# Performance work log

Hardware: AMD Instinct MI355X
Metric: run time of the kernel (lower is better)

Reference implementation:

```python
import math
import jax, jax.numpy as jnp
import numpy as np

N_HEADS = 16


def setup_inputs() -> dict:
    key = jax.random.key(0)
    k1, k2 = jax.random.split(key)
    qkv = jax.random.normal(k1, (2, 3072, 2048), dtype=jnp.float32)
    mask = jax.random.randint(k2, (2, 1, 2048), 0, 2).astype(jnp.bool_)
    return {"qkv": qkv, "mask": mask}


def reference(qkv, mask):
    bs, width, length = qkv.shape
    ch = width // (3 * N_HEADS)
    q, k, v = jnp.split(qkv, 3, axis=1)  # each [bs, H*C, T]
    scale = 1.0 / math.sqrt(math.sqrt(ch))  # applied to both q and k
    q = (q * scale).reshape(bs * N_HEADS, ch, length)
    k = (k * scale).reshape(bs * N_HEADS, ch, length)
    # [B*H, T, T] scores
    weight = jnp.einsum('bct,bcs->bts', q, k)
    # mask: [bs, 1, T] bool, True = valid token
    inv = ~mask[:, 0, :]                      # [bs, T]
    pad = inv[:, None, :] | inv[:, :, None]   # [bs, T, T]
    pad = jnp.broadcast_to(pad[:, None], (bs, N_HEADS, length, length))
    pad = pad.reshape(bs * N_HEADS, length, length)
    weight = jnp.where(pad, jnp.finfo(weight.dtype).min, weight)
    weight = jax.nn.softmax(weight.astype(jnp.float32), axis=-1).astype(qkv.dtype)
    a = jnp.einsum('bts,bcs->bct', weight, v.reshape(bs * N_HEADS, ch, length))
    return a.reshape(bs, N_HEADS * ch, length)
```

## Files before the change

kernel.cpp:

```cpp
#include <hip/hip_runtime.h>
#include <float.h>


typedef __attribute__((ext_vector_type(8))) short bf16x8;
typedef __attribute__((ext_vector_type(4))) float f32x4;

#define TSEQ 2048
#define QT_OFF 0L
#define KT_OFF 4194304L
#define VB_OFF 8388608L

#if __has_builtin(__builtin_amdgcn_exp2f)
#define EXPFN(x) __builtin_amdgcn_exp2f(x)
#define SM_SCALE (0.125f * 1.44269504088896f)
#else
#define EXPFN(x) __expf(x)
#define SM_SCALE 0.125f
#endif

__device__ inline short f2bf(float x) {
    union { float f; unsigned u; } un; un.f = x;
    unsigned r = un.u + 0x7fffu + ((un.u >> 16) & 1u);
    return (short)(r >> 16);
}

__device__ inline unsigned pkbf(float a, float b) {
    unsigned au = __float_as_uint(a) + 0x8000u;
    unsigned bu = __float_as_uint(b) + 0x8000u;
    return __builtin_amdgcn_perm(bu, au, 0x07060302u);
}

__global__ __launch_bounds__(256) void prep_kernel(
    const float* __restrict__ qkv, short* __restrict__ ws)
{
    const int tid = threadIdx.x;
    const int job = blockIdx.x;
    if (job < 2048) {
        __shared__ float Ls[64 * 65];
        const int which = job & 1;
        const int rest  = job >> 1;
        const int bh = rest & 31;
        const int tt = rest >> 5;
        const int b = bh >> 4, h = bh & 15;
        const float* src = qkv + (long)b * 6291456 + ((long)(which * 1024 + h * 64)) * TSEQ + tt * 64;
        short* dst = ws + (which ? KT_OFF : QT_OFF) + ((long)bh * TSEQ + tt * 64) * 64;
        const float scale = which ? 1.0f : SM_SCALE;
        #pragma unroll
        for (int ch = 0; ch < 4; ++ch) {
            int idx = tid + ch * 256;
            int c = idx >> 4, tch = idx & 15;
            float4 v = *(const float4*)(src + (long)c * TSEQ + tch * 4);
            float* L = &Ls[c * 65 + tch * 4];
            L[0] = v.x; L[1] = v.y; L[2] = v.z; L[3] = v.w;
        }
        __syncthreads();
        #pragma unroll
        for (int ch = 0; ch < 2; ++ch) {
            int idx = tid + ch * 256;
            int t = idx >> 3, cch = idx & 7;
            bf16x8 o;
            #pragma unroll
            for (int j = 0; j < 8; ++j)
                o[j] = f2bf(Ls[(cch * 8 + j) * 65 + t] * scale);
            *(bf16x8*)(dst + (long)t * 64 + cch * 8) = o;
        }
    } else {
        const int v = job - 2048;
        #pragma unroll
        for (int ch = 0; ch < 4; ++ch) {
            long i = (long)v * 4096 + tid * 4 + ch * 1024;
            long b = i >> 21, r = i & 2097151;
            float4 x = *(const float4*)(qkv + b * 6291456 + 4194304 + r);
            short4 o;
            o.x = f2bf(x.x); o.y = f2bf(x.y); o.z = f2bf(x.z); o.w = f2bf(x.w);
            *(short4*)(ws + VB_OFF + i) = o;
        }
    }
}

__global__ __launch_bounds__(256, 2) void attn_kernel(
    const short* __restrict__ ws, const int* __restrict__ mask,
    float* __restrict__ out)
{
    __shared__ __align__(16) char smem[63488];
    short* Ps  = (short*)smem;
    float* mbf = (float*)(smem + 55296);
    float* Os  = (float*)smem;

    const int tid  = threadIdx.x;
    const int lane = tid & 63, wid = tid >> 6;
    const int l15  = lane & 15, quad = lane >> 4;
    const int srow = tid >> 3, scch = tid & 7;

    const int blk  = blockIdx.x;
    const int head = blk & 31;
    const int qt   = blk >> 5;
    const int b    = head >> 4, h = head & 15;
    const int t0   = qt * 128;

    const short* Qt = ws + QT_OFF + (long)head * TSEQ * 64;
    const short* Kt = ws + KT_OFF + (long)head * TSEQ * 64;
    const short* Vg = ws + VB_OFF + (long)head * 64 * TSEQ;
    const long obase = ((long)b * 1024 + h * 64) * TSEQ;

    for (int i = tid; i < TSEQ; i += 256)
        mbf[i] = (mask[b * TSEQ + i] != 0) ? 0.0f : -1e30f;

    #pragma unroll
    for (int ch = 0; ch < 4; ++ch) {
        int row = srow + ch * 32;
        *(bf16x8*)&Ps[row * 72 + scch * 8] =
            *(const bf16x8*)(Qt + (long)(t0 + row) * 64 + scch * 8);
    }
    #pragma unroll
    for (int ch = 0; ch < 2; ++ch) {
        int row = srow + ch * 32;
        *(bf16x8*)(smem + 18432 + (row * 72 + scch * 8) * 2) =
            *(const bf16x8*)(Kt + (long)row * 64 + scch * 8);
        *(bf16x8*)(smem + 36864 + (row * 72 + scch * 8) * 2) =
            *(const bf16x8*)(Vg + (long)row * TSEQ + scch * 8);
    }
    __syncthreads();

    bf16x8 qb[2][2];
    #pragma unroll
    for (int nt = 0; nt < 2; ++nt)
        #pragma unroll
        for (int hf = 0; hf < 2; ++hf)
            qb[nt][hf] = *(const bf16x8*)&Ps[(wid * 32 + nt * 16 + l15) * 72 + quad * 8 + hf * 32];
    bool qv[2];
    #pragma unroll
    for (int nt = 0; nt < 2; ++nt)
        qv[nt] = (mbf[t0 + wid * 32 + nt * 16 + l15] != 0.0f);

    float l_s[2] = {0.0f, 0.0f};
    f32x4 Oacc[2][4];
    #pragma unroll
    for (int mt = 0; mt < 2; ++mt)
        #pragma unroll
        for (int nc = 0; nc < 4; ++nc)
            #pragma unroll
            for (int r = 0; r < 4; ++r) Oacc[mt][nc][r] = 0.0f;

    short* Pw = Ps + wid * 32 * 72;
    int p = 0;

    for (int it = 0; it < 32; ++it) {
        const int s0 = it * 64;
        const int sn = ((it + 1) & 31) * 64;
        short* Kb = (short*)(smem + 18432 + p * 9216);
        short* Vb = (short*)(smem + 36864 + p * 9216);
        short* Kn = (short*)(smem + 18432 + (1 - p) * 9216);
        short* Vn = (short*)(smem + 36864 + (1 - p) * 9216);

        bf16x8 kst[2], vst[2];
        #pragma unroll
        for (int ch = 0; ch < 2; ++ch) {
            int row = srow + ch * 32;
            kst[ch] = *(const bf16x8*)(Kt + (long)(sn + row) * 64 + scch * 8);
            vst[ch] = *(const bf16x8*)(Vg + (long)row * TSEQ + sn + scch * 8);
        }

        f32x4 bias[4];
        #pragma unroll
        for (int ns = 0; ns < 4; ++ns)
            bias[ns] = *(const f32x4*)&mbf[s0 + ns * 16 + quad * 4];

        f32x4 Sacc[4][2];
        #pragma unroll
        for (int ns = 0; ns < 4; ++ns) {
            bf16x8 ka0 = *(const bf16x8*)&Kb[(ns * 16 + l15) * 72 + quad * 8];
            bf16x8 ka1 = *(const bf16x8*)&Kb[(ns * 16 + l15) * 72 + quad * 8 + 32];
            #pragma unroll
            for (int nt = 0; nt < 2; ++nt) {
                Sacc[ns][nt] = __builtin_amdgcn_mfma_f32_16x16x32_bf16(
                    ka0, qb[nt][0], bias[ns], 0, 0, 0);
                Sacc[ns][nt] = __builtin_amdgcn_mfma_f32_16x16x32_bf16(
                    ka1, qb[nt][1], Sacc[ns][nt], 0, 0, 0);
            }
        }

        #pragma unroll
        for (int nt = 0; nt < 2; ++nt) {
            float ls = 0.0f;
            #pragma unroll
            for (int ns = 0; ns < 4; ++ns) {
                float pv[4];
                #pragma unroll
                for (int r = 0; r < 4; ++r) {
                    float e = EXPFN(Sacc[ns][nt][r]);
                    pv[r] = qv[nt] ? 1.0f : e;
                    ls += pv[r];
                }
                uint2 pk;
                pk.x = pkbf(pv[0], pv[1]);
                pk.y = pkbf(pv[2], pv[3]);
                *(uint2*)&Pw[(nt * 16 + l15) * 72 + ns * 16 + quad * 4] = pk;
            }
            ls += __shfl_xor(ls, 16);
            ls += __shfl_xor(ls, 32);
            l_s[nt] += ls;
        }

        bf16x8 pa[2][2];
        #pragma unroll
        for (int mt = 0; mt < 2; ++mt)
            #pragma unroll
            for (int hf = 0; hf < 2; ++hf)
                pa[mt][hf] = *(const bf16x8*)&Pw[(mt * 16 + l15) * 72 + quad * 8 + hf * 32];
        #pragma unroll
        for (int hf = 0; hf < 2; ++hf)
            #pragma unroll
            for (int nc = 0; nc < 4; ++nc) {
                bf16x8 vb = *(const bf16x8*)&Vb[(nc * 16 + l15) * 72 + quad * 8 + hf * 32];
                #pragma unroll
                for (int mt = 0; mt < 2; ++mt)
                    Oacc[mt][nc] = __builtin_amdgcn_mfma_f32_16x16x32_bf16(
                        pa[mt][hf], vb, Oacc[mt][nc], 0, 0, 0);
            }

        #pragma unroll
        for (int ch = 0; ch < 2; ++ch) {
            int row = srow + ch * 32;
            *(bf16x8*)&Kn[row * 72 + scch * 8] = kst[ch];
            *(bf16x8*)&Vn[row * 72 + scch * 8] = vst[ch];
        }
        __syncthreads();
        p ^= 1;
    }

    float inv[2];
    #pragma unroll
    for (int nt = 0; nt < 2; ++nt) inv[nt] = 1.0f / l_s[nt];
    float iw[2][4];
    #pragma unroll
    for (int mt = 0; mt < 2; ++mt)
        #pragma unroll
        for (int r = 0; r < 4; ++r)
            iw[mt][r] = __shfl(inv[mt], 4 * quad + r);
    #pragma unroll
    for (int mt = 0; mt < 2; ++mt)
        #pragma unroll
        for (int nc = 0; nc < 4; ++nc) {
            float4 o;
            o.x = Oacc[mt][nc][0] * iw[mt][0];
            o.y = Oacc[mt][nc][1] * iw[mt][1];
            o.z = Oacc[mt][nc][2] * iw[mt][2];
            o.w = Oacc[mt][nc][3] * iw[mt][3];
            *(float4*)&Os[(nc * 16 + l15) * 132 + wid * 32 + mt * 16 + quad * 4] = o;
        }
    __syncthreads();
    #pragma unroll
    for (int ch = 0; ch < 8; ++ch) {
        int idx = tid + ch * 256;
        int c = idx >> 5, tch = idx & 31;
        *(float4*)(out + obase + (long)c * TSEQ + t0 + tch * 4) =
            *(const float4*)&Os[c * 132 + tch * 4];
    }
}

extern "C" void kernel_launch(void* const* d_in, const int* in_sizes, int n_in,
                              void* d_out, int out_size, void* d_ws, size_t ws_size,
                              hipStream_t stream) {
    const float* qkv  = (const float*)d_in[0];
    const int*   mask = (const int*)d_in[1];
    float*       out  = (float*)d_out;
    short*       ws   = (short*)d_ws;
    prep_kernel<<<dim3(3072), dim3(256), 0, stream>>>(qkv, ws);
    attn_kernel<<<dim3(512), dim3(256), 0, stream>>>(ws, mask, out);
}
```

Baseline: 150.3 us.

## Load K/V MFMA fragments directly from global into registers, drop LDS staging

Removes the shared-memory double-buffered K and V tiles and the per-iteration block barrier. Each wave now reads its Q, K and V MFMA fragments straight from global memory into registers, with K for the next tile prefetched in registers. LDS use drops to the per-wave P scratch and the mask bias, which could allow more blocks per CU. In exchange every wave redundantly fetches the same K/V data from L1/L2 rather than sharing it through LDS. Register pressure also rises from holding the prefetched fragments.

```diff
diff --git a/kernel.cpp b/kernel.cpp
--- a/kernel.cpp
+++ b/kernel.cpp
@@ -82,15 +82,14 @@
     const short* __restrict__ ws, const int* __restrict__ mask,
     float* __restrict__ out)
 {
-    __shared__ __align__(16) char smem[63488];
+    __shared__ __align__(16) char smem[33792];
     short* Ps  = (short*)smem;
-    float* mbf = (float*)(smem + 55296);
+    float* mbf = (float*)(smem + 18432);
     float* Os  = (float*)smem;
 
     const int tid  = threadIdx.x;
     const int lane = tid & 63, wid = tid >> 6;
     const int l15  = lane & 15, quad = lane >> 4;
-    const int srow = tid >> 3, scch = tid & 7;
 
     const int blk  = blockIdx.x;
     const int head = blk & 31;
@@ -105,21 +104,6 @@
 
     for (int i = tid; i < TSEQ; i += 256)
         mbf[i] = (mask[b * TSEQ + i] != 0) ? 0.0f : -1e30f;
-
-    #pragma unroll
-    for (int ch = 0; ch < 4; ++ch) {
-        int row = srow + ch * 32;
-        *(bf16x8*)&Ps[row * 72 + scch * 8] =
-            *(const bf16x8*)(Qt + (long)(t0 + row) * 64 + scch * 8);
-    }
-    #pragma unroll
-    for (int ch = 0; ch < 2; ++ch) {
-        int row = srow + ch * 32;
-        *(bf16x8*)(smem + 18432 + (row * 72 + scch * 8) * 2) =
-            *(const bf16x8*)(Kt + (long)row * 64 + scch * 8);
-        *(bf16x8*)(smem + 36864 + (row * 72 + scch * 8) * 2) =
-            *(const bf16x8*)(Vg + (long)row * TSEQ + scch * 8);
-    }
     __syncthreads();
 
     bf16x8 qb[2][2];
@@ -127,7 +111,8 @@
     for (int nt = 0; nt < 2; ++nt)
         #pragma unroll
         for (int hf = 0; hf < 2; ++hf)
-            qb[nt][hf] = *(const bf16x8*)&Ps[(wid * 32 + nt * 16 + l15) * 72 + quad * 8 + hf * 32];
+            qb[nt][hf] = *(const bf16x8*)(Qt +
+                (long)(t0 + wid * 32 + nt * 16 + l15) * 64 + quad * 8 + hf * 32);
     bool qv[2];
     #pragma unroll
     for (int nt = 0; nt < 2; ++nt)
@@ -143,23 +128,33 @@
             for (int r = 0; r < 4; ++r) Oacc[mt][nc][r] = 0.0f;
 
     short* Pw = Ps + wid * 32 * 72;
-    int p = 0;
+
+    bf16x8 kf[4][2];
+    #pragma unroll
+    for (int ns = 0; ns < 4; ++ns)
+        #pragma unroll
+        for (int hf = 0; hf < 2; ++hf)
+            kf[ns][hf] = *(const bf16x8*)(Kt +
+                (long)(ns * 16 + l15) * 64 + quad * 8 + hf * 32);
 
     for (int it = 0; it < 32; ++it) {
         const int s0 = it * 64;
         const int sn = ((it + 1) & 31) * 64;
-        short* Kb = (short*)(smem + 18432 + p * 9216);
-        short* Vb = (short*)(smem + 36864 + p * 9216);
-        short* Kn = (short*)(smem + 18432 + (1 - p) * 9216);
-        short* Vn = (short*)(smem + 36864 + (1 - p) * 9216);
-
-        bf16x8 kst[2], vst[2];
-        #pragma unroll
-        for (int ch = 0; ch < 2; ++ch) {
-            int row = srow + ch * 32;
-            kst[ch] = *(const bf16x8*)(Kt + (long)(sn + row) * 64 + scch * 8);
-            vst[ch] = *(const bf16x8*)(Vg + (long)row * TSEQ + sn + scch * 8);
-        }
+
+        bf16x8 vf[4][2];
+        #pragma unroll
+        for (int nc = 0; nc < 4; ++nc)
+            #pragma unroll
+            for (int hf = 0; hf < 2; ++hf)
+                vf[nc][hf] = *(const bf16x8*)(Vg +
+                    (long)(nc * 16 + l15) * TSEQ + s0 + quad * 8 + hf * 32);
+        bf16x8 kn[4][2];
+        #pragma unroll
+        for (int ns = 0; ns < 4; ++ns)
+            #pragma unroll
+            for (int hf = 0; hf < 2; ++hf)
+                kn[ns][hf] = *(const bf16x8*)(Kt +
+                    (long)(sn + ns * 16 + l15) * 64 + quad * 8 + hf * 32);
 
         f32x4 bias[4];
         #pragma unroll
@@ -168,17 +163,14 @@
 
         f32x4 Sacc[4][2];
         #pragma unroll
-        for (int ns = 0; ns < 4; ++ns) {
-            bf16x8 ka0 = *(const bf16x8*)&Kb[(ns * 16 + l15) * 72 + quad * 8];
-            bf16x8 ka1 = *(const bf16x8*)&Kb[(ns * 16 + l15) * 72 + quad * 8 + 32];
+        for (int ns = 0; ns < 4; ++ns)
             #pragma unroll
             for (int nt = 0; nt < 2; ++nt) {
                 Sacc[ns][nt] = __builtin_amdgcn_mfma_f32_16x16x32_bf16(
-                    ka0, qb[nt][0], bias[ns], 0, 0, 0);
+                    kf[ns][0], qb[nt][0], bias[ns], 0, 0, 0);
                 Sacc[ns][nt] = __builtin_amdgcn_mfma_f32_16x16x32_bf16(
-                    ka1, qb[nt][1], Sacc[ns][nt], 0, 0, 0);
+                    kf[ns][1], qb[nt][1], Sacc[ns][nt], 0, 0, 0);
             }
-        }
 
         #pragma unroll
         for (int nt = 0; nt < 2; ++nt) {
@@ -211,24 +203,20 @@
         #pragma unroll
         for (int hf = 0; hf < 2; ++hf)
             #pragma unroll
-            for (int nc = 0; nc < 4; ++nc) {
-                bf16x8 vb = *(const bf16x8*)&Vb[(nc * 16 + l15) * 72 + quad * 8 + hf * 32];
+            for (int nc = 0; nc < 4; ++nc)
                 #pragma unroll
                 for (int mt = 0; mt < 2; ++mt)
                     Oacc[mt][nc] = __builtin_amdgcn_mfma_f32_16x16x32_bf16(
-                        pa[mt][hf], vb, Oacc[mt][nc], 0, 0, 0);
-            }
-
-        #pragma unroll
-        for (int ch = 0; ch < 2; ++ch) {
-            int row = srow + ch * 32;
-            *(bf16x8*)&Kn[row * 72 + scch * 8] = kst[ch];
-            *(bf16x8*)&Vn[row * 72 + scch * 8] = vst[ch];
-        }
-        __syncthreads();
-        p ^= 1;
+                        pa[mt][hf], vf[nc][hf], Oacc[mt][nc], 0, 0, 0);
+
+        #pragma unroll
+        for (int ns = 0; ns < 4; ++ns)
+            #pragma unroll
+            for (int hf = 0; hf < 2; ++hf)
+                kf[ns][hf] = kn[ns][hf];
     }
 
+    __syncthreads();
     float inv[2];
     #pragma unroll
     for (int nt = 0; nt < 2; ++nt) inv[nt] = 1.0f / l_s[nt];
```

Measured after the change: 211.0 us. 1.4x slower.
